# Performance work log

Measured on AMD Instinct MI355X. Metric: run time of the kernel, lower is better.

The kernel has to match this reference:

```python
import jax, jax.numpy as jnp
import numpy as np

B, T, D, NH = 2, 2048, 2048, 16
HID = D  # hidden_dim must equal emb_dim for the source's fc2(x1) to type-check
HD = D // NH
EPS = 1e-5


def setup_inputs() -> dict:
    key = jax.random.key(0)
    ks = jax.random.split(key, 16)
    s = 0.02
    inp = {
        "x": jax.random.normal(ks[0], (B, T, D), jnp.float32),
        "Wq": jax.random.normal(ks[1], (D, D), jnp.float32) * s,
        "bq": jnp.zeros((D,), jnp.float32),
        "Wk": jax.random.normal(ks[2], (D, D), jnp.float32) * s,
        "bk": jnp.zeros((D,), jnp.float32),
        "Wv": jax.random.normal(ks[3], (D, D), jnp.float32) * s,
        "bv": jnp.zeros((D,), jnp.float32),
        "Wo": jax.random.normal(ks[4], (D, D), jnp.float32) * s,
        "bo": jnp.zeros((D,), jnp.float32),
        "scale1": jnp.ones((D,), jnp.float32),
        "scale2": jnp.ones((D,), jnp.float32),
        "W1": jax.random.normal(ks[5], (D, HID), jnp.float32) * s,
        "W2": jax.random.normal(ks[6], (D, HID), jnp.float32) * s,  # fc2: Linear(emb_dim, hidden_dim)
        "W3": jax.random.normal(ks[7], (HID, D), jnp.float32) * s,
    }
    return inp


def _rmsnorm(x, scale):
    m = jnp.mean(x * x, axis=-1, keepdims=True)
    return scale * (x * jax.lax.rsqrt(m + EPS))


def _attention(x, Wq, bq, Wk, bk, Wv, bv, Wo, bo):
    b, t, _ = x.shape
    q = (x @ Wq + bq).reshape(b, t, NH, HD)
    k = (x @ Wk + bk).reshape(b, t, NH, HD)
    v = (x @ Wv + bv).reshape(b, t, NH, HD)
    # energy: [B, H, T, T]; softmax over keys, scaled by 1/sqrt(head_dim); NO causal mask in source
    energy = jnp.einsum("bqhd,bkhd->bhqk", q, k) / jnp.sqrt(jnp.float32(HD))
    attn = jax.nn.softmax(energy, axis=-1)
    out = jnp.einsum("bhqk,bkhd->bqhd", attn, v).reshape(b, t, D)
    return out @ Wo + bo


def _ffn(x, W1, W2, W3):
    x1 = x @ W1                       # [B,T,HID]
    x2 = x1 @ W2                      # source quirk: fc2 applied to x1 (hidden_dim == emb_dim)
    return (x1 * jax.nn.sigmoid(x1) * x2) @ W3


def reference(x, Wq, bq, Wk, bk, Wv, bv, Wo, bo, scale1, scale2, W1, W2, W3):
    shortcut = x
    h = _rmsnorm(x, scale1)
    h = _attention(h, Wq, bq, Wk, bk, Wv, bv, Wo, bo)
    h = shortcut + h
    h = _rmsnorm(h, scale2)
    h = _ffn(h, W1, W2, W3)
    # source adds the ORIGINAL input again (shortcut never reassigned)
    return h + shortcut
```

## Files before the change

### kernel.cpp

```cpp
#include <hip/hip_runtime.h>

typedef __bf16 bf16x8 __attribute__((ext_vector_type(8)));
typedef __bf16 bf16x4v __attribute__((ext_vector_type(4)));
typedef float  f32x4  __attribute__((ext_vector_type(4)));

#define LDS_AS(p) ((__attribute__((address_space(3))) void*)(p))
#define GLB_AS(p) ((const __attribute__((address_space(1))) void*)(p))

static __device__ inline unsigned short bfbits(__bf16 x) {
  union { __bf16 b; unsigned short u; } c; c.b = x; return c.u;
}

struct TP { const float* s[7]; __bf16* d[7]; };
__global__ __launch_bounds__(256) void transpose_convert_all(TP p) {
  const float* __restrict__ W = p.s[blockIdx.z];
  __bf16* __restrict__ Wt = p.d[blockIdx.z];
  __shared__ float tile[32][33];
  const int tx = threadIdx.x & 31, ty = threadIdx.x >> 5;
  const int n0 = blockIdx.x * 32, k0 = blockIdx.y * 32;
#pragma unroll
  for (int j = 0; j < 4; ++j)
    tile[ty + j * 8][tx] = W[(size_t)(k0 + ty + j * 8) * 2048 + n0 + tx];
  __syncthreads();
#pragma unroll
  for (int j = 0; j < 4; ++j)
    Wt[(size_t)(n0 + ty + j * 8) * 2048 + k0 + tx] = (__bf16)tile[tx][ty + j * 8];
}

__global__ __launch_bounds__(256) void rmsnorm_k(
    const float* __restrict__ x, const float* __restrict__ scale,
    __bf16* __restrict__ out) {
  const int row = blockIdx.x, t = threadIdx.x;
  const float4* xr = (const float4*)(x + (size_t)row * 2048);
  float4 a = xr[t], b2 = xr[t + 256];
  float ss = a.x * a.x + a.y * a.y + a.z * a.z + a.w * a.w +
             b2.x * b2.x + b2.y * b2.y + b2.z * b2.z + b2.w * b2.w;
#pragma unroll
  for (int ofs = 32; ofs; ofs >>= 1) ss += __shfl_xor(ss, ofs, 64);
  __shared__ float red[4];
  if ((t & 63) == 0) red[t >> 6] = ss;
  __syncthreads();
  ss = red[0] + red[1] + red[2] + red[3];
  const float rs = rsqrtf(ss * (1.f / 2048.f) + 1e-5f);
  const float4* sr = (const float4*)scale;
  float4 s1 = sr[t], s2 = sr[t + 256];
  __bf16* orow = out + (size_t)row * 2048;
  orow[t * 4 + 0] = (__bf16)(a.x * rs * s1.x);
  orow[t * 4 + 1] = (__bf16)(a.y * rs * s1.y);
  orow[t * 4 + 2] = (__bf16)(a.z * rs * s1.z);
  orow[t * 4 + 3] = (__bf16)(a.w * rs * s1.w);
  orow[(t + 256) * 4 + 0] = (__bf16)(b2.x * rs * s2.x);
  orow[(t + 256) * 4 + 1] = (__bf16)(b2.y * rs * s2.y);
  orow[(t + 256) * 4 + 2] = (__bf16)(b2.z * rs * s2.z);
  orow[(t + 256) * 4 + 3] = (__bf16)(b2.w * rs * s2.w);
}

template <bool OUTF32, bool HASBIAS, bool HASRES, bool SILU, bool TRANSV>
__global__ __launch_bounds__(256) void gemm_bt(
    const __bf16* __restrict__ A, const __bf16* __restrict__ Bt,
    const float* __restrict__ bias, const float* __restrict__ res,
    const __bf16* __restrict__ ew, void* __restrict__ Cout,
    int M, int N, int Kd) {
  __shared__ __attribute__((aligned(16))) __bf16 As[128 * 32];
  __shared__ __attribute__((aligned(16))) __bf16 Bs[128 * 32];
  const int tid = threadIdx.x;
  const int w = tid >> 6, l = tid & 63;
  const int M0 = blockIdx.y * 128, N0 = blockIdx.x * 128;
  const int wr = w >> 1, wc = w & 1;
  const int lm = l & 15, lq = l >> 4;

  f32x4 acc[4][4];
#pragma unroll
  for (int mt = 0; mt < 4; ++mt)
#pragma unroll
    for (int nt = 0; nt < 4; ++nt)
#pragma unroll
      for (int e = 0; e < 4; ++e) acc[mt][nt][e] = 0.f;

  const int offA0 = (w * 2 + 0) * 1024 + l * 16;
  const int offA1 = (w * 2 + 1) * 1024 + l * 16;
  const int row0 = offA0 >> 6, kb0 = offA0 & 63;
  const int row1 = offA1 >> 6, kb1 = offA1 & 63;

  for (int k0 = 0; k0 < Kd; k0 += 32) {
    {
      const char* ga0 = (const char*)(A + (size_t)(M0 + row0) * Kd + k0) + kb0;
      const char* ga1 = (const char*)(A + (size_t)(M0 + row1) * Kd + k0) + kb1;
      const char* gb0 = (const char*)(Bt + (size_t)(N0 + row0) * Kd + k0) + kb0;
      const char* gb1 = (const char*)(Bt + (size_t)(N0 + row1) * Kd + k0) + kb1;
      __builtin_amdgcn_global_load_lds(GLB_AS(ga0), LDS_AS(((char*)As) + (w * 2 + 0) * 1024), 16, 0, 0);
      __builtin_amdgcn_global_load_lds(GLB_AS(ga1), LDS_AS(((char*)As) + (w * 2 + 1) * 1024), 16, 0, 0);
      __builtin_amdgcn_global_load_lds(GLB_AS(gb0), LDS_AS(((char*)Bs) + (w * 2 + 0) * 1024), 16, 0, 0);
      __builtin_amdgcn_global_load_lds(GLB_AS(gb1), LDS_AS(((char*)Bs) + (w * 2 + 1) * 1024), 16, 0, 0);
    }
    __syncthreads();
    bf16x8 af[4], bfr[4];
#pragma unroll
    for (int mt = 0; mt < 4; ++mt)
      af[mt] = *(const bf16x8*)(As + (wr * 64 + mt * 16 + lm) * 32 + lq * 8);
#pragma unroll
    for (int nt = 0; nt < 4; ++nt)
      bfr[nt] = *(const bf16x8*)(Bs + (wc * 64 + nt * 16 + lm) * 32 + lq * 8);
#pragma unroll
    for (int mt = 0; mt < 4; ++mt)
#pragma unroll
      for (int nt = 0; nt < 4; ++nt)
        acc[mt][nt] = __builtin_amdgcn_mfma_f32_16x16x32_bf16(af[mt], bfr[nt], acc[mt][nt], 0, 0, 0);
    __syncthreads();
  }

  const int lr = lq * 4;
#pragma unroll
  for (int mt = 0; mt < 4; ++mt) {
#pragma unroll
    for (int nt = 0; nt < 4; ++nt) {
      const int col = N0 + wc * 64 + nt * 16 + lm;
      float bv = 0.f;
      if (HASBIAS) bv = bias[col];
      if (TRANSV) {
        const int rw0 = M0 + wr * 64 + mt * 16 + lr;
        const int bidx = rw0 >> 11, tok = rw0 & 2047;
        bf16x4v pk;
#pragma unroll
        for (int i = 0; i < 4; ++i) pk[i] = (__bf16)(acc[mt][nt][i] + bv);
        *(bf16x4v*)((__bf16*)Cout + ((size_t)(bidx * 2048 + col)) * 2048 + tok) = pk;
      } else {
#pragma unroll
        for (int i = 0; i < 4; ++i) {
          const int row = M0 + wr * 64 + mt * 16 + lr + i;
          const size_t off = (size_t)row * N + col;
          float v = acc[mt][nt][i] + bv;
          if (HASRES) v += res[off];
          if (SILU) {
            const float x1v = (float)ew[off];
            v = x1v * (1.f / (1.f + __expf(-x1v))) * v;
          }
          if (OUTF32) ((float*)Cout)[off] = v;
          else ((__bf16*)Cout)[off] = (__bf16)v;
        }
      }
    }
  }
}

__global__ __launch_bounds__(256, 2) void attn_mfma(
    const __bf16* __restrict__ Q, const __bf16* __restrict__ K,
    const __bf16* __restrict__ Vt, __bf16* __restrict__ O) {
  __shared__ __attribute__((aligned(16))) char KsL[16 * 1024];
  __shared__ __attribute__((aligned(16))) char VsL[16 * 1024];
  __shared__ __attribute__((aligned(16))) char PbL[16 * 1024];

  const int t = threadIdx.x;
  const int w = t >> 6, l = t & 63;
  const int lm = l & 15, quad = l >> 4;
  const int h = blockIdx.y, b = blockIdx.z;
  const int q0 = blockIdx.x * 128;
  const size_t Ds = 2048;
  const size_t hoff = (size_t)h * 128;
  const size_t bbase = (size_t)b * 2048;
  const int sl16 = ((lm << 2) | quad) * 16;
  const float SC = 0.08838834764831845f;

  bf16x8 qf[2][4];
#pragma unroll
  for (int ntq = 0; ntq < 2; ++ntq)
#pragma unroll
    for (int ks = 0; ks < 4; ++ks)
      qf[ntq][ks] = *(const bf16x8*)(Q + (bbase + q0 + w * 32 + ntq * 16 + lm) * Ds + hoff + ks * 32 + quad * 8);

  f32x4 oacc[2][8];
#pragma unroll
  for (int mtq = 0; mtq < 2; ++mtq)
#pragma unroll
    for (int nv = 0; nv < 8; ++nv)
#pragma unroll
      for (int e = 0; e < 4; ++e) oacc[mtq][nv][e] = 0.f;
  float lpart[2] = {0.f, 0.f};

  char* Pw = PbL + w * 4096;
  const int krow = l >> 2;
  const int kcol = (l & 3) * 8;

  for (int kt = 0; kt < 2048; kt += 64) {
    __syncthreads();
#pragma unroll
    for (int i = 0; i < 4; ++i) {
      const __bf16* src = K + (bbase + kt + i * 16 + krow) * Ds + hoff + w * 32 + kcol;
      __builtin_amdgcn_global_load_lds(GLB_AS(src), LDS_AS(KsL + (i * 4 + w) * 1024), 16, 0, 0);
    }
#pragma unroll
    for (int i = 0; i < 4; ++i) {
      const int c = i * 4 + w;
      const __bf16* src = Vt + (bbase + hoff + (c >> 1) * 16 + krow) * Ds + kt + (c & 1) * 32 + kcol;
      __builtin_amdgcn_global_load_lds(GLB_AS(src), LDS_AS(VsL + c * 1024), 16, 0, 0);
    }
    __syncthreads();

    f32x4 st[4][2];
#pragma unroll
    for (int mtk = 0; mtk < 4; ++mtk)
#pragma unroll
      for (int ntq = 0; ntq < 2; ++ntq)
#pragma unroll
        for (int e = 0; e < 4; ++e) st[mtk][ntq][e] = 0.f;
#pragma unroll
    for (int ks = 0; ks < 4; ++ks) {
#pragma unroll
      for (int mtk = 0; mtk < 4; ++mtk) {
        bf16x8 kf = *(const bf16x8*)(KsL + (mtk * 4 + ks) * 1024 + sl16);
        st[mtk][0] = __builtin_amdgcn_mfma_f32_16x16x32_bf16(kf, qf[0][ks], st[mtk][0], 0, 0, 0);
        st[mtk][1] = __builtin_amdgcn_mfma_f32_16x16x32_bf16(kf, qf[1][ks], st[mtk][1], 0, 0, 0);
      }
    }

#pragma unroll
    for (int mtk = 0; mtk < 4; ++mtk) {
#pragma unroll
      for (int ntq = 0; ntq < 2; ++ntq) {
        unsigned int pk0, pk1;
        {
          const float p0 = __expf(st[mtk][ntq][0] * SC);
          const float p1 = __expf(st[mtk][ntq][1] * SC);
          const float p2 = __expf(st[mtk][ntq][2] * SC);
          const float p3 = __expf(st[mtk][ntq][3] * SC);
          const __bf16 b0 = (__bf16)p0, b1 = (__bf16)p1, b2 = (__bf16)p2, b3 = (__bf16)p3;
          lpart[ntq] += (float)b0 + (float)b1 + (float)b2 + (float)b3;
          pk0 = (unsigned int)bfbits(b0) | ((unsigned int)bfbits(b1) << 16);
          pk1 = (unsigned int)bfbits(b2) | ((unsigned int)bfbits(b3) << 16);
        }
        const int chunk = ntq * 2 + (mtk >> 1);
        const int slot = (lm << 2) | (((mtk & 1) << 1) | (quad >> 1));
        uint2* dst = (uint2*)(Pw + chunk * 1024 + slot * 16 + (quad & 1) * 8);
        *dst = make_uint2(pk0, pk1);
      }
    }

#pragma unroll
    for (int k2 = 0; k2 < 2; ++k2) {
      bf16x8 p0 = *(const bf16x8*)(Pw + (0 * 2 + k2) * 1024 + sl16);
      bf16x8 p1 = *(const bf16x8*)(Pw + (1 * 2 + k2) * 1024 + sl16);
#pragma unroll
      for (int nv = 0; nv < 8; ++nv) {
        bf16x8 vf = *(const bf16x8*)(VsL + (nv * 2 + k2) * 1024 + sl16);
        oacc[0][nv] = __builtin_amdgcn_mfma_f32_16x16x32_bf16(p0, vf, oacc[0][nv], 0, 0, 0);
        oacc[1][nv] = __builtin_amdgcn_mfma_f32_16x16x32_bf16(p1, vf, oacc[1][nv], 0, 0, 0);
      }
    }
  }

  float linv[2];
#pragma unroll
  for (int ntq = 0; ntq < 2; ++ntq) {
    float v = lpart[ntq];
    v += __shfl_xor(v, 16, 64);
    v += __shfl_xor(v, 32, 64);
    linv[ntq] = 1.f / v;
  }
  float oinv[2][4];
#pragma unroll
  for (int mtq = 0; mtq < 2; ++mtq)
#pragma unroll
    for (int r = 0; r < 4; ++r)
      oinv[mtq][r] = __shfl(linv[mtq], quad * 4 + r, 64);

#pragma unroll
  for (int mtq = 0; mtq < 2; ++mtq)
#pragma unroll
    for (int nv = 0; nv < 8; ++nv)
#pragma unroll
      for (int r = 0; r < 4; ++r) {
        const int qrow = q0 + w * 32 + mtq * 16 + quad * 4 + r;
        O[(bbase + qrow) * Ds + hoff + nv * 16 + lm] = (__bf16)(oacc[mtq][nv][r] * oinv[mtq][r]);
      }
}

extern "C" void kernel_launch(void* const* d_in, const int* in_sizes, int n_in,
                              void* d_out, int out_size, void* d_ws, size_t ws_size,
                              hipStream_t stream) {
  const float* x      = (const float*)d_in[0];
  const float* Wq     = (const float*)d_in[1];
  const float* bq     = (const float*)d_in[2];
  const float* Wk     = (const float*)d_in[3];
  const float* bk     = (const float*)d_in[4];
  const float* Wv     = (const float*)d_in[5];
  const float* bv     = (const float*)d_in[6];
  const float* Wo     = (const float*)d_in[7];
  const float* bo     = (const float*)d_in[8];
  const float* scale1 = (const float*)d_in[9];
  const float* scale2 = (const float*)d_in[10];
  const float* W1     = (const float*)d_in[11];
  const float* W2     = (const float*)d_in[12];
  const float* W3     = (const float*)d_in[13];

  const int M = 4096, N = 2048, Kd = 2048;
  char* ws = (char*)d_ws;
  const size_t WT_B = (size_t)2048 * 2048 * 2;
  const size_t ACT_B = (size_t)4096 * 2048 * 2;
  __bf16* wt[7];
  size_t off = 0;
  for (int i = 0; i < 7; ++i) { wt[i] = (__bf16*)(ws + off); off += WT_B; }
  __bf16* hn1  = (__bf16*)(ws + off); off += ACT_B;
  __bf16* Qb   = (__bf16*)(ws + off); off += ACT_B;
  __bf16* Kb   = (__bf16*)(ws + off); off += ACT_B;
  __bf16* VtG  = (__bf16*)(ws + off); off += ACT_B;
  __bf16* attn = (__bf16*)(ws + off); off += ACT_B;
  __bf16* hn2  = (__bf16*)(ws + off); off += ACT_B;
  __bf16* x1b  = (__bf16*)(ws + off); off += ACT_B;
  __bf16* fmb  = (__bf16*)(ws + off); off += ACT_B;

  dim3 tb(256);
  {
    TP p;
    p.s[0] = Wq; p.s[1] = Wk; p.s[2] = Wv; p.s[3] = Wo; p.s[4] = W1; p.s[5] = W2; p.s[6] = W3;
    for (int i = 0; i < 7; ++i) p.d[i] = wt[i];
    transpose_convert_all<<<dim3(64, 64, 7), tb, 0, stream>>>(p);
  }

  rmsnorm_k<<<4096, tb, 0, stream>>>(x, scale1, hn1);

  dim3 gg(N / 128, M / 128);
  gemm_bt<false, true, false, false, false><<<gg, tb, 0, stream>>>(hn1, wt[0], bq, nullptr, nullptr, Qb, M, N, Kd);
  gemm_bt<false, true, false, false, false><<<gg, tb, 0, stream>>>(hn1, wt[1], bk, nullptr, nullptr, Kb, M, N, Kd);
  gemm_bt<false, true, false, false, true ><<<gg, tb, 0, stream>>>(hn1, wt[2], bv, nullptr, nullptr, VtG, M, N, Kd);

  dim3 ag(2048 / 128, 16, 2);
  attn_mfma<<<ag, tb, 0, stream>>>(Qb, Kb, VtG, attn);

  gemm_bt<true, true, true, false, false><<<gg, tb, 0, stream>>>(attn, wt[3], bo, x, nullptr, d_out, M, N, Kd);

  rmsnorm_k<<<4096, tb, 0, stream>>>((const float*)d_out, scale2, hn2);

  gemm_bt<false, false, false, false, false><<<gg, tb, 0, stream>>>(hn2, wt[4], nullptr, nullptr, nullptr, x1b, M, N, Kd);
  gemm_bt<false, false, false, true, false><<<gg, tb, 0, stream>>>(x1b, wt[5], nullptr, nullptr, x1b, fmb, M, N, Kd);
  gemm_bt<true, false, true, false, false><<<gg, tb, 0, stream>>>(fmb, wt[6], nullptr, x, nullptr, d_out, M, N, Kd);
}
```

Before: 695.8 us.

## Double-buffer GEMM and attention tiles, fuse QKV GEMM, keep P in registers

New measurement: 649.2 us. 6.7% less time.

```diff
diff --git a/kernel.cpp b/kernel.cpp
--- a/kernel.cpp
+++ b/kernel.cpp
@@ -6,10 +6,6 @@
 
 #define LDS_AS(p) ((__attribute__((address_space(3))) void*)(p))
 #define GLB_AS(p) ((const __attribute__((address_space(1))) void*)(p))
-
-static __device__ inline unsigned short bfbits(__bf16 x) {
-  union { __bf16 b; unsigned short u; } c; c.b = x; return c.u;
-}
 
 struct TP { const float* s[7]; __bf16* d[7]; };
 __global__ __launch_bounds__(256) void transpose_convert_all(TP p) {
@@ -55,14 +51,14 @@
   orow[(t + 256) * 4 + 3] = (__bf16)(b2.w * rs * s2.w);
 }
 
-template <bool OUTF32, bool HASBIAS, bool HASRES, bool SILU, bool TRANSV>
+template <bool OUTF32, bool HASBIAS, bool HASRES, bool SILU>
 __global__ __launch_bounds__(256) void gemm_bt(
     const __bf16* __restrict__ A, const __bf16* __restrict__ Bt,
     const float* __restrict__ bias, const float* __restrict__ res,
     const __bf16* __restrict__ ew, void* __restrict__ Cout,
     int M, int N, int Kd) {
-  __shared__ __attribute__((aligned(16))) __bf16 As[128 * 32];
-  __shared__ __attribute__((aligned(16))) __bf16 Bs[128 * 32];
+  __shared__ __attribute__((aligned(16))) __bf16 As[2][128 * 32];
+  __shared__ __attribute__((aligned(16))) __bf16 Bs[2][128 * 32];
   const int tid = threadIdx.x;
   const int w = tid >> 6, l = tid & 63;
   const int M0 = blockIdx.y * 128, N0 = blockIdx.x * 128;
@@ -81,32 +77,37 @@
   const int offA1 = (w * 2 + 1) * 1024 + l * 16;
   const int row0 = offA0 >> 6, kb0 = offA0 & 63;
   const int row1 = offA1 >> 6, kb1 = offA1 & 63;
-
-  for (int k0 = 0; k0 < Kd; k0 += 32) {
-    {
-      const char* ga0 = (const char*)(A + (size_t)(M0 + row0) * Kd + k0) + kb0;
-      const char* ga1 = (const char*)(A + (size_t)(M0 + row1) * Kd + k0) + kb1;
-      const char* gb0 = (const char*)(Bt + (size_t)(N0 + row0) * Kd + k0) + kb0;
-      const char* gb1 = (const char*)(Bt + (size_t)(N0 + row1) * Kd + k0) + kb1;
-      __builtin_amdgcn_global_load_lds(GLB_AS(ga0), LDS_AS(((char*)As) + (w * 2 + 0) * 1024), 16, 0, 0);
-      __builtin_amdgcn_global_load_lds(GLB_AS(ga1), LDS_AS(((char*)As) + (w * 2 + 1) * 1024), 16, 0, 0);
-      __builtin_amdgcn_global_load_lds(GLB_AS(gb0), LDS_AS(((char*)Bs) + (w * 2 + 0) * 1024), 16, 0, 0);
-      __builtin_amdgcn_global_load_lds(GLB_AS(gb1), LDS_AS(((char*)Bs) + (w * 2 + 1) * 1024), 16, 0, 0);
-    }
+  const int nIt = Kd >> 5;
+
+  auto stage = [&](int k0, int bsel) {
+    const char* ga0 = (const char*)(A + (size_t)(M0 + row0) * Kd + k0) + kb0;
+    const char* ga1 = (const char*)(A + (size_t)(M0 + row1) * Kd + k0) + kb1;
+    const char* gb0 = (const char*)(Bt + (size_t)(N0 + row0) * Kd + k0) + kb0;
+    const char* gb1 = (const char*)(Bt + (size_t)(N0 + row1) * Kd + k0) + kb1;
+    __builtin_amdgcn_global_load_lds(GLB_AS(ga0), LDS_AS(((char*)As[bsel]) + (w * 2 + 0) * 1024), 16, 0, 0);
+    __builtin_amdgcn_global_load_lds(GLB_AS(ga1), LDS_AS(((char*)As[bsel]) + (w * 2 + 1) * 1024), 16, 0, 0);
+    __builtin_amdgcn_global_load_lds(GLB_AS(gb0), LDS_AS(((char*)Bs[bsel]) + (w * 2 + 0) * 1024), 16, 0, 0);
+    __builtin_amdgcn_global_load_lds(GLB_AS(gb1), LDS_AS(((char*)Bs[bsel]) + (w * 2 + 1) * 1024), 16, 0, 0);
+  };
+
+  stage(0, 0);
+  for (int it = 0; it < nIt; ++it) {
     __syncthreads();
+    if (it + 1 < nIt) stage((it + 1) * 32, (it + 1) & 1);
+    const __bf16* Ab = As[it & 1];
+    const __bf16* Bb = Bs[it & 1];
     bf16x8 af[4], bfr[4];
 #pragma unroll
     for (int mt = 0; mt < 4; ++mt)
-      af[mt] = *(const bf16x8*)(As + (wr * 64 + mt * 16 + lm) * 32 + lq * 8);
+      af[mt] = *(const bf16x8*)(Ab + (wr * 64 + mt * 16 + lm) * 32 + lq * 8);
 #pragma unroll
     for (int nt = 0; nt < 4; ++nt)
-      bfr[nt] = *(const bf16x8*)(Bs + (wc * 64 + nt * 16 + lm) * 32 + lq * 8);
+      bfr[nt] = *(const bf16x8*)(Bb + (wc * 64 + nt * 16 + lm) * 32 + lq * 8);
 #pragma unroll
     for (int mt = 0; mt < 4; ++mt)
 #pragma unroll
       for (int nt = 0; nt < 4; ++nt)
         acc[mt][nt] = __builtin_amdgcn_mfma_f32_16x16x32_bf16(af[mt], bfr[nt], acc[mt][nt], 0, 0, 0);
-    __syncthreads();
   }
 
   const int lr = lq * 4;
@@ -117,27 +118,114 @@
       const int col = N0 + wc * 64 + nt * 16 + lm;
       float bv = 0.f;
       if (HASBIAS) bv = bias[col];
-      if (TRANSV) {
+#pragma unroll
+      for (int i = 0; i < 4; ++i) {
+        const int row = M0 + wr * 64 + mt * 16 + lr + i;
+        const size_t off = (size_t)row * N + col;
+        float v = acc[mt][nt][i] + bv;
+        if (HASRES) v += res[off];
+        if (SILU) {
+          const float x1v = (float)ew[off];
+          v = x1v * (1.f / (1.f + __expf(-x1v))) * v;
+        }
+        if (OUTF32) ((float*)Cout)[off] = v;
+        else ((__bf16*)Cout)[off] = (__bf16)v;
+      }
+    }
+  }
+}
+
+__global__ __launch_bounds__(256) void gemm_qkv(
+    const __bf16* __restrict__ A, const __bf16* __restrict__ Bt,
+    const float* __restrict__ bq, const float* __restrict__ bk,
+    const float* __restrict__ bv,
+    __bf16* __restrict__ Qout, __bf16* __restrict__ Kout,
+    __bf16* __restrict__ Vtout, int Kd) {
+  __shared__ __attribute__((aligned(16))) __bf16 As[2][128 * 32];
+  __shared__ __attribute__((aligned(16))) __bf16 Bs[2][128 * 32];
+  const int tid = threadIdx.x;
+  const int w = tid >> 6, l = tid & 63;
+  const int M0 = blockIdx.y * 128, N0 = blockIdx.x * 128;
+  const int wr = w >> 1, wc = w & 1;
+  const int lm = l & 15, lq = l >> 4;
+
+  f32x4 acc[4][4];
+#pragma unroll
+  for (int mt = 0; mt < 4; ++mt)
+#pragma unroll
+    for (int nt = 0; nt < 4; ++nt)
+#pragma unroll
+      for (int e = 0; e < 4; ++e) acc[mt][nt][e] = 0.f;
+
+  const int offA0 = (w * 2 + 0) * 1024 + l * 16;
+  const int offA1 = (w * 2 + 1) * 1024 + l * 16;
+  const int row0 = offA0 >> 6, kb0 = offA0 & 63;
+  const int row1 = offA1 >> 6, kb1 = offA1 & 63;
+  const int nIt = Kd >> 5;
+
+  auto stage = [&](int k0, int bsel) {
+    const char* ga0 = (const char*)(A + (size_t)(M0 + row0) * Kd + k0) + kb0;
+    const char* ga1 = (const char*)(A + (size_t)(M0 + row1) * Kd + k0) + kb1;
+    const char* gb0 = (const char*)(Bt + (size_t)(N0 + row0) * Kd + k0) + kb0;
+    const char* gb1 = (const char*)(Bt + (size_t)(N0 + row1) * Kd + k0) + kb1;
+    __builtin_amdgcn_global_load_lds(GLB_AS(ga0), LDS_AS(((char*)As[bsel]) + (w * 2 + 0) * 1024), 16, 0, 0);
+    __builtin_amdgcn_global_load_lds(GLB_AS(ga1), LDS_AS(((char*)As[bsel]) + (w * 2 + 1) * 1024), 16, 0, 0);
+    __builtin_amdgcn_global_load_lds(GLB_AS(gb0), LDS_AS(((char*)Bs[bsel]) + (w * 2 + 0) * 1024), 16, 0, 0);
+    __builtin_amdgcn_global_load_lds(GLB_AS(gb1), LDS_AS(((char*)Bs[bsel]) + (w * 2 + 1) * 1024), 16, 0, 0);
+  };
+
+  stage(0, 0);
+  for (int it = 0; it < nIt; ++it) {
+    __syncthreads();
+    if (it + 1 < nIt) stage((it + 1) * 32, (it + 1) & 1);
+    const __bf16* Ab = As[it & 1];
+    const __bf16* Bb = Bs[it & 1];
+    bf16x8 af[4], bfr[4];
+#pragma unroll
+    for (int mt = 0; mt < 4; ++mt)
+      af[mt] = *(const bf16x8*)(Ab + (wr * 64 + mt * 16 + lm) * 32 + lq * 8);
+#pragma unroll
+    for (int nt = 0; nt < 4; ++nt)
+      bfr[nt] = *(const bf16x8*)(Bb + (wc * 64 + nt * 16 + lm) * 32 + lq * 8);
+#pragma unroll
+    for (int mt = 0; mt < 4; ++mt)
+#pragma unroll
+      for (int nt = 0; nt < 4; ++nt)
+        acc[mt][nt] = __builtin_amdgcn_mfma_f32_16x16x32_bf16(af[mt], bfr[nt], acc[mt][nt], 0, 0, 0);
+  }
+
+  const int lr = lq * 4;
+  const int seg = N0 >> 11;
+  const int nbase = N0 & 2047;
+  const float* bb = (seg == 0) ? bq : ((seg == 1) ? bk : bv);
+  if (seg < 2) {
+    __bf16* dst = (seg == 0) ? Qout : Kout;
+#pragma unroll
+    for (int mt = 0; mt < 4; ++mt) {
+#pragma unroll
+      for (int nt = 0; nt < 4; ++nt) {
+        const int col = nbase + wc * 64 + nt * 16 + lm;
+        const float bvv = bb[col];
+#pragma unroll
+        for (int i = 0; i < 4; ++i) {
+          const int row = M0 + wr * 64 + mt * 16 + lr + i;
+          dst[(size_t)row * 2048 + col] = (__bf16)(acc[mt][nt][i] + bvv);
+        }
+      }
+    }
+  } else {
+#pragma unroll
+    for (int mt = 0; mt < 4; ++mt) {
+#pragma unroll
+      for (int nt = 0; nt < 4; ++nt) {
+        const int col = nbase + wc * 64 + nt * 16 + lm;
+        const float bvv = bb[col];
         const int rw0 = M0 + wr * 64 + mt * 16 + lr;
         const int bidx = rw0 >> 11, tok = rw0 & 2047;
         bf16x4v pk;
 #pragma unroll
-        for (int i = 0; i < 4; ++i) pk[i] = (__bf16)(acc[mt][nt][i] + bv);
-        *(bf16x4v*)((__bf16*)Cout + ((size_t)(bidx * 2048 + col)) * 2048 + tok) = pk;
-      } else {
-#pragma unroll
-        for (int i = 0; i < 4; ++i) {
-          const int row = M0 + wr * 64 + mt * 16 + lr + i;
-          const size_t off = (size_t)row * N + col;
-          float v = acc[mt][nt][i] + bv;
-          if (HASRES) v += res[off];
-          if (SILU) {
-            const float x1v = (float)ew[off];
-            v = x1v * (1.f / (1.f + __expf(-x1v))) * v;
-          }
-          if (OUTF32) ((float*)Cout)[off] = v;
-          else ((__bf16*)Cout)[off] = (__bf16)v;
-        }
+        for (int i = 0; i < 4; ++i) pk[i] = (__bf16)(acc[mt][nt][i] + bvv);
+        *(bf16x4v*)(Vtout + ((size_t)(bidx * 2048 + col)) * 2048 + tok) = pk;
       }
     }
   }
@@ -146,9 +234,8 @@
 __global__ __launch_bounds__(256, 2) void attn_mfma(
     const __bf16* __restrict__ Q, const __bf16* __restrict__ K,
     const __bf16* __restrict__ Vt, __bf16* __restrict__ O) {
-  __shared__ __attribute__((aligned(16))) char KsL[16 * 1024];
-  __shared__ __attribute__((aligned(16))) char VsL[16 * 1024];
-  __shared__ __attribute__((aligned(16))) char PbL[16 * 1024];
+  __shared__ __attribute__((aligned(16))) char KsL[2][16 * 1024];
+  __shared__ __attribute__((aligned(16))) char VsL[2][16 * 1024];
 
   const int t = threadIdx.x;
   const int w = t >> 6, l = t & 63;
@@ -159,7 +246,10 @@
   const size_t hoff = (size_t)h * 128;
   const size_t bbase = (size_t)b * 2048;
   const int sl16 = ((lm << 2) | quad) * 16;
-  const float SC = 0.08838834764831845f;
+  const float SCL = 0.08838834764831845f * 1.4426950408889634f;
+
+  const int krow = l >> 2, kcol = (l & 3) * 8;
+  const int vth = l & 3, vd = l >> 2;
 
   bf16x8 qf[2][4];
 #pragma unroll
@@ -170,31 +260,53 @@
 
   f32x4 oacc[2][8];
 #pragma unroll
-  for (int mtq = 0; mtq < 2; ++mtq)
+  for (int ntq = 0; ntq < 2; ++ntq)
 #pragma unroll
     for (int nv = 0; nv < 8; ++nv)
 #pragma unroll
-      for (int e = 0; e < 4; ++e) oacc[mtq][nv][e] = 0.f;
+      for (int e = 0; e < 4; ++e) oacc[ntq][nv][e] = 0.f;
   float lpart[2] = {0.f, 0.f};
 
-  char* Pw = PbL + w * 4096;
-  const int krow = l >> 2;
-  const int kcol = (l & 3) * 8;
-
-  for (int kt = 0; kt < 2048; kt += 64) {
-    __syncthreads();
+  bf16x8 vreg[4];
+
+  auto loadV = [&](int kt) {
+#pragma unroll
+    for (int i = 0; i < 4; ++i) {
+      const int chunk = w * 4 + i;
+      const int nv = chunk >> 1, c = chunk & 1;
+      vreg[i] = *(const bf16x8*)(Vt + (bbase + hoff + nv * 16 + vd) * Ds + kt + c * 32 + vth * 8);
+    }
+  };
+  auto stageK = [&](int kt, char* Kb) {
 #pragma unroll
     for (int i = 0; i < 4; ++i) {
       const __bf16* src = K + (bbase + kt + i * 16 + krow) * Ds + hoff + w * 32 + kcol;
-      __builtin_amdgcn_global_load_lds(GLB_AS(src), LDS_AS(KsL + (i * 4 + w) * 1024), 16, 0, 0);
-    }
+      __builtin_amdgcn_global_load_lds(GLB_AS(src), LDS_AS(Kb + (i * 4 + w) * 1024), 16, 0, 0);
+    }
+  };
+  auto writeV = [&](char* Vb) {
+    const int s0off = ((vd << 2) | ((vth & 1) * 2)) * 16 + (vth >> 1) * 8;
 #pragma unroll
     for (int i = 0; i < 4; ++i) {
-      const int c = i * 4 + w;
-      const __bf16* src = Vt + (bbase + hoff + (c >> 1) * 16 + krow) * Ds + kt + (c & 1) * 32 + kcol;
-      __builtin_amdgcn_global_load_lds(GLB_AS(src), LDS_AS(VsL + c * 1024), 16, 0, 0);
-    }
+      char* base = Vb + (w * 4 + i) * 1024;
+      uint4 u = *(const uint4*)&vreg[i];
+      *(uint2*)(base + s0off) = make_uint2(u.x, u.y);
+      *(uint2*)(base + s0off + 16) = make_uint2(u.z, u.w);
+    }
+  };
+
+  loadV(0);
+  stageK(0, KsL[0]);
+  writeV(VsL[0]);
+
+  for (int it = 0; it < 32; ++it) {
     __syncthreads();
+    const int cur = it & 1;
+    const bool more = (it + 1) < 32;
+    if (more) { loadV((it + 1) * 64); stageK((it + 1) * 64, KsL[(it + 1) & 1]); }
+
+    const char* Kb = KsL[cur];
+    const char* Vb = VsL[cur];
 
     f32x4 st[4][2];
 #pragma unroll
@@ -207,45 +319,38 @@
     for (int ks = 0; ks < 4; ++ks) {
 #pragma unroll
       for (int mtk = 0; mtk < 4; ++mtk) {
-        bf16x8 kf = *(const bf16x8*)(KsL + (mtk * 4 + ks) * 1024 + sl16);
+        bf16x8 kf = *(const bf16x8*)(Kb + (mtk * 4 + ks) * 1024 + sl16);
         st[mtk][0] = __builtin_amdgcn_mfma_f32_16x16x32_bf16(kf, qf[0][ks], st[mtk][0], 0, 0, 0);
         st[mtk][1] = __builtin_amdgcn_mfma_f32_16x16x32_bf16(kf, qf[1][ks], st[mtk][1], 0, 0, 0);
       }
     }
 
 #pragma unroll
-    for (int mtk = 0; mtk < 4; ++mtk) {
+    for (int c = 0; c < 2; ++c) {
+      bf16x8 pf[2];
 #pragma unroll
       for (int ntq = 0; ntq < 2; ++ntq) {
-        unsigned int pk0, pk1;
-        {
-          const float p0 = __expf(st[mtk][ntq][0] * SC);
-          const float p1 = __expf(st[mtk][ntq][1] * SC);
-          const float p2 = __expf(st[mtk][ntq][2] * SC);
-          const float p3 = __expf(st[mtk][ntq][3] * SC);
-          const __bf16 b0 = (__bf16)p0, b1 = (__bf16)p1, b2 = (__bf16)p2, b3 = (__bf16)p3;
-          lpart[ntq] += (float)b0 + (float)b1 + (float)b2 + (float)b3;
-          pk0 = (unsigned int)bfbits(b0) | ((unsigned int)bfbits(b1) << 16);
-          pk1 = (unsigned int)bfbits(b2) | ((unsigned int)bfbits(b3) << 16);
+#pragma unroll
+        for (int half = 0; half < 2; ++half) {
+          const f32x4 sv = st[c * 2 + half][ntq];
+#pragma unroll
+          for (int r = 0; r < 4; ++r) {
+            const float p = exp2f(sv[r] * SCL);
+            const __bf16 pb = (__bf16)p;
+            pf[ntq][half * 4 + r] = pb;
+            lpart[ntq] += (float)pb;
+          }
         }
-        const int chunk = ntq * 2 + (mtk >> 1);
-        const int slot = (lm << 2) | (((mtk & 1) << 1) | (quad >> 1));
-        uint2* dst = (uint2*)(Pw + chunk * 1024 + slot * 16 + (quad & 1) * 8);
-        *dst = make_uint2(pk0, pk1);
-      }
-    }
-
-#pragma unroll
-    for (int k2 = 0; k2 < 2; ++k2) {
-      bf16x8 p0 = *(const bf16x8*)(Pw + (0 * 2 + k2) * 1024 + sl16);
-      bf16x8 p1 = *(const bf16x8*)(Pw + (1 * 2 + k2) * 1024 + sl16);
+      }
 #pragma unroll
       for (int nv = 0; nv < 8; ++nv) {
-        bf16x8 vf = *(const bf16x8*)(VsL + (nv * 2 + k2) * 1024 + sl16);
-        oacc[0][nv] = __builtin_amdgcn_mfma_f32_16x16x32_bf16(p0, vf, oacc[0][nv], 0, 0, 0);
-        oacc[1][nv] = __builtin_amdgcn_mfma_f32_16x16x32_bf16(p1, vf, oacc[1][nv], 0, 0, 0);
-      }
-    }
+        bf16x8 vf = *(const bf16x8*)(Vb + (nv * 2 + c) * 1024 + sl16);
+        oacc[0][nv] = __builtin_amdgcn_mfma_f32_16x16x32_bf16(pf[0], vf, oacc[0][nv], 0, 0, 0);
+        oacc[1][nv] = __builtin_amdgcn_mfma_f32_16x16x32_bf16(pf[1], vf, oacc[1][nv], 0, 0, 0);
+      }
+    }
+
+    if (more) writeV(VsL[(it + 1) & 1]);
   }
 
   float linv[2];
@@ -258,19 +363,19 @@
   }
   float oinv[2][4];
 #pragma unroll
-  for (int mtq = 0; mtq < 2; ++mtq)
+  for (int ntq = 0; ntq < 2; ++ntq)
 #pragma unroll
     for (int r = 0; r < 4; ++r)
-      oinv[mtq][r] = __shfl(linv[mtq], quad * 4 + r, 64);
-
-#pragma unroll
-  for (int mtq = 0; mtq < 2; ++mtq)
+      oinv[ntq][r] = __shfl(linv[ntq], quad * 4 + r, 64);
+
+#pragma unroll
+  for (int ntq = 0; ntq < 2; ++ntq)
 #pragma unroll
     for (int nv = 0; nv < 8; ++nv)
 #pragma unroll
       for (int r = 0; r < 4; ++r) {
-        const int qrow = q0 + w * 32 + mtq * 16 + quad * 4 + r;
-        O[(bbase + qrow) * Ds + hoff + nv * 16 + lm] = (__bf16)(oacc[mtq][nv][r] * oinv[mtq][r]);
+        const int qrow = q0 + w * 32 + ntq * 16 + quad * 4 + r;
+        O[(bbase + qrow) * Ds + hoff + nv * 16 + lm] = (__bf16)(oacc[ntq][nv][r] * oinv[ntq][r]);
       }
 }
 
@@ -318,19 +423,18 @@
 
   rmsnorm_k<<<4096, tb, 0, stream>>>(x, scale1, hn1);
 
-  dim3 gg(N / 128, M / 128);
-  gemm_bt<false, true, false, false, false><<<gg, tb, 0, stream>>>(hn1, wt[0], bq, nullptr, nullptr, Qb, M, N, Kd);
-  gemm_bt<false, true, false, false, false><<<gg, tb, 0, stream>>>(hn1, wt[1], bk, nullptr, nullptr, Kb, M, N, Kd);
-  gemm_bt<false, true, false, false, true ><<<gg, tb, 0, stream>>>(hn1, wt[2], bv, nullptr, nullptr, VtG, M, N, Kd);
+  gemm_qkv<<<dim3(6144 / 128, M / 128), tb, 0, stream>>>(
+      hn1, wt[0], bq, bk, bv, Qb, Kb, VtG, Kd);
 
   dim3 ag(2048 / 128, 16, 2);
   attn_mfma<<<ag, tb, 0, stream>>>(Qb, Kb, VtG, attn);
 
-  gemm_bt<true, true, true, false, false><<<gg, tb, 0, stream>>>(attn, wt[3], bo, x, nullptr, d_out, M, N, Kd);
+  dim3 gg(N / 128, M / 128);
+  gemm_bt<true, true, true, false><<<gg, tb, 0, stream>>>(attn, wt[3], bo, x, nullptr, d_out, M, N, Kd);
 
   rmsnorm_k<<<4096, tb, 0, stream>>>((const float*)d_out, scale2, hn2);
 
-  gemm_bt<false, false, false, false, false><<<gg, tb, 0, stream>>>(hn2, wt[4], nullptr, nullptr, nullptr, x1b, M, N, Kd);
-  gemm_bt<false, false, false, true, false><<<gg, tb, 0, stream>>>(x1b, wt[5], nullptr, nullptr, x1b, fmb, M, N, Kd);
-  gemm_bt<true, false, true, false, false><<<gg, tb, 0, stream>>>(fmb, wt[6], nullptr, x, nullptr, d_out, M, N, Kd);
-}
+  gemm_bt<false, false, false, false><<<gg, tb, 0, stream>>>(hn2, wt[4], nullptr, nullptr, nullptr, x1b, M, N, Kd);
+  gemm_bt<false, false, false, true><<<gg, tb, 0, stream>>>(x1b, wt[5], nullptr, nullptr, x1b, fmb, M, N, Kd);
+  gemm_bt<true, false, true, false><<<gg, tb, 0, stream>>>(fmb, wt[6], nullptr, x, nullptr, d_out, M, N, Kd);
+}
```
